# Optimization experiments

Hardware: AMD Instinct MI355X
Metric: run time of the kernel (lower is better)

Reference implementation:

```python
import jax, jax.numpy as jnp
import numpy as np
import math

S, B, H, NH = 2048, 1, 4096, 32
D = H // NH  # 128 head dim


def rotate_half(x):
    x1, x2 = x[..., : x.shape[-1] // 2], x[..., x.shape[-1] // 2 :]
    return jnp.concatenate((-x2, x1), axis=-1)


def setup_inputs() -> dict:
    key = jax.random.key(0)
    k1, k2, k3, k4, k5 = jax.random.split(key, 5)
    hidden_states = jax.random.normal(k1, (S, B, H), dtype=jnp.float32)
    position_ids = jnp.broadcast_to(jnp.arange(S, dtype=jnp.int32)[None, :], (B, S))
    # causal mask: True = masked (upper triangle above diagonal)
    attention_mask = jnp.triu(jnp.ones((S, S), dtype=bool), k=1)[None, None]
    W_qkv = jax.random.normal(k2, (H, 3 * H), dtype=jnp.float32) * 0.02
    b_qkv = jax.random.normal(k3, (3 * H,), dtype=jnp.float32) * 0.02
    W_dense = jax.random.normal(k4, (H, H), dtype=jnp.float32) * 0.02
    b_dense = jax.random.normal(k5, (H,), dtype=jnp.float32) * 0.02
    return {
        "hidden_states": hidden_states,
        "position_ids": position_ids,
        "attention_mask": attention_mask,
        "W_qkv": W_qkv,
        "b_qkv": b_qkv,
        "W_dense": W_dense,
        "b_dense": b_dense,
        "layer_id": 27,
    }


def reference(hidden_states, position_ids, attention_mask, W_qkv, b_qkv, W_dense, b_dense, layer_id):
    s, b, h = hidden_states.shape
    nh, d = NH, D
    # QKV projection: [s, b, 3h] -> [s, b, nh, 3d] -> split
    mixed = hidden_states @ W_qkv + b_qkv
    mixed = mixed.reshape(s, b, nh, 3 * d)
    q, k, v = jnp.split(mixed, 3, axis=-1)  # each [s, b, nh, d]
    # rotary embedding indexed by position_ids (transposed to [s, b])
    pos = position_ids.T  # [s, b]
    inv_freq = 1.0 / (10000.0 ** (jnp.arange(0, d, 2, dtype=jnp.float32) / d))
    freqs = pos[..., None].astype(jnp.float32) * inv_freq  # [s, b, d/2]
    emb = jnp.concatenate((freqs, freqs), axis=-1)  # [s, b, d]
    cos = jnp.cos(emb)[:, :, None, :]  # [s, b, 1, d]
    sin = jnp.sin(emb)[:, :, None, :]
    q = q * cos + rotate_half(q) * sin
    k = k * cos + rotate_half(k) * sin
    # attention with per-layer scaling coeff (cancels in softmax except mask fill)
    coeff = jnp.float32(layer_id + 1)
    q_scaled = q / (math.sqrt(d) * coeff)
    scores = jnp.einsum("sbnd,tbnd->bnst", q_scaled, k)  # [b, nh, s, s]
    scores = jnp.where(attention_mask, jnp.float32(-10000.0), scores) * coeff
    probs = jax.nn.softmax(scores, axis=-1)
    ctx = jnp.einsum("bnst,tbnd->sbnd", probs, v).reshape(s, b, h)
    out = ctx @ W_dense + b_dense
    return out
```

## Files before the change

kernel.cpp:

```cpp
#include <hip/hip_runtime.h>

#define S_LEN 2048
#define HID   4096
#define NHEAD 32
#define DHEAD 128
#define H3    12288

typedef __attribute__((ext_vector_type(8))) __bf16 bf16x8;
typedef __attribute__((ext_vector_type(4))) __bf16 bf16x4;
typedef __attribute__((ext_vector_type(4))) float  f32x4;

__device__ __forceinline__ void gl_lds16(const void* g, void* l) {
  __builtin_amdgcn_global_load_lds(
      (const __attribute__((address_space(1))) void*)g,
      (__attribute__((address_space(3))) void*)l, 16, 0, 0);
}

__global__ void cvt_f32_bf16(const float* __restrict__ in, __bf16* __restrict__ out, int n4) {
  int i = blockIdx.x * blockDim.x + threadIdx.x;
  if (i >= n4) return;
  float4 v = ((const float4*)in)[i];
  bf16x4 o;
  o.x = (__bf16)v.x; o.y = (__bf16)v.y; o.z = (__bf16)v.z; o.w = (__bf16)v.w;
  ((bf16x4*)out)[i] = o;
}

__global__ void transpose_cvt(const float* __restrict__ in, __bf16* __restrict__ out, int R, int C) {
  __shared__ float t[64][65];
  const int tid = threadIdx.x;
  const int r0 = blockIdx.y * 64, c0 = blockIdx.x * 64;
#pragma unroll
  for (int p = 0; p < 4; ++p) {
    int r = p * 16 + (tid >> 4);
    int c4 = (tid & 15) * 4;
    float4 v = *(const float4*)(in + (size_t)(r0 + r) * C + c0 + c4);
    t[r][c4] = v.x; t[r][c4 + 1] = v.y; t[r][c4 + 2] = v.z; t[r][c4 + 3] = v.w;
  }
  __syncthreads();
#pragma unroll
  for (int p = 0; p < 4; ++p) {
    int c = p * 16 + (tid >> 4);
    int rg = (tid & 15) * 4;
    bf16x4 o;
    o.x = (__bf16)t[rg][c]; o.y = (__bf16)t[rg + 1][c];
    o.z = (__bf16)t[rg + 2][c]; o.w = (__bf16)t[rg + 3][c];
    *(bf16x4*)(out + (size_t)(c0 + c) * R + r0 + rg) = o;
  }
}

__global__ void rope_kernel(__bf16* __restrict__ q, __bf16* __restrict__ k,
                            const int* __restrict__ pos) {
  int idx = blockIdx.x * 256 + threadIdx.x;
  int j = idx & 63;
  int hs = idx >> 6;
  int s = hs & (S_LEN - 1);
  float p = (float)pos[s];
  float invf = __expf(-(float)j * (9.210340371976184f / 64.f));
  float a = p * invf;
  float c, sn;
  __sincosf(a, &sn, &c);
  size_t base = (size_t)hs * 128;
  float x1 = (float)q[base + j], x2 = (float)q[base + j + 64];
  q[base + j]      = (__bf16)(x1 * c - x2 * sn);
  q[base + j + 64] = (__bf16)(x2 * c + x1 * sn);
  x1 = (float)k[base + j]; x2 = (float)k[base + j + 64];
  k[base + j]      = (__bf16)(x1 * c - x2 * sn);
  k[base + j + 64] = (__bf16)(x2 * c + x1 * sn);
}

template <int EPI>
__global__ __launch_bounds__(256, 2)
void gemm_bf16(const __bf16* __restrict__ A, const __bf16* __restrict__ BT,
               const float* __restrict__ bias, int K,
               __bf16* __restrict__ outq, __bf16* __restrict__ outk,
               __bf16* __restrict__ outvt, float* __restrict__ outf) {
  const int tid = threadIdx.x;
  const int lane = tid & 63;
  const int wave = tid >> 6;
  const int bm = blockIdx.x * 128;
  const int bn = blockIdx.y * 128;

  __shared__ __bf16 As[128 * 64];
  __shared__ __bf16 Bs[128 * 64];
  char* Ab = (char*)As;
  char* Bb = (char*)Bs;

  f32x4 acc[4][4] = {};

  const int wm = (wave >> 1) * 64;
  const int wn = (wave & 1) * 64;

  const int sr = tid >> 3;
  const int sc = (tid & 7) * 16;
  const int scs = sc ^ ((sr & 7) << 4);

  const char* Arow = (const char*)(A + (size_t)(bm + sr) * K) + scs;
  const char* Brow = (const char*)(BT + (size_t)(bn + sr) * K) + scs;

  for (int k0 = 0; k0 < K; k0 += 64) {
    const char* a_src = Arow + (size_t)k0 * 2;
    const char* b_src = Brow + (size_t)k0 * 2;
    char* a_dst = Ab + wave * 1024;
    char* b_dst = Bb + wave * 1024;
#pragma unroll
    for (int i = 0; i < 4; ++i) {
      gl_lds16(a_src + (size_t)i * 32 * K * 2, a_dst + i * 4096);
      gl_lds16(b_src + (size_t)i * 32 * K * 2, b_dst + i * 4096);
    }
    __syncthreads();
#pragma unroll
    for (int kk = 0; kk < 2; ++kk) {
      bf16x8 af[4], bfr[4];
#pragma unroll
      for (int m = 0; m < 4; ++m) {
        int row = wm + m * 16 + (lane & 15);
        int cb = (kk * 64 + ((lane >> 4) << 4)) ^ ((row & 7) << 4);
        af[m] = *(const bf16x8*)(Ab + row * 128 + cb);
      }
#pragma unroll
      for (int n = 0; n < 4; ++n) {
        int row = wn + n * 16 + (lane & 15);
        int cb = (kk * 64 + ((lane >> 4) << 4)) ^ ((row & 7) << 4);
        bfr[n] = *(const bf16x8*)(Bb + row * 128 + cb);
      }
#pragma unroll
      for (int m = 0; m < 4; ++m)
#pragma unroll
        for (int n = 0; n < 4; ++n)
          acc[m][n] = __builtin_amdgcn_mfma_f32_16x16x32_bf16(af[m], bfr[n], acc[m][n], 0, 0, 0);
    }
    __syncthreads();
  }

  const int rbase = (lane >> 4) << 2;
  const int cl = lane & 15;
  if (EPI == 0) {
    const int route = (bn >> 7) % 3;
    const int head = bn / 384;
#pragma unroll
    for (int n = 0; n < 4; ++n) {
      const int d = wn + n * 16 + cl;
      const float bv = bias[bn + d];
#pragma unroll
      for (int m = 0; m < 4; ++m) {
        const int srow = bm + wm + m * 16 + rbase;
        if (route == 2) {
          bf16x4 o;
          o.x = (__bf16)(acc[m][n][0] + bv);
          o.y = (__bf16)(acc[m][n][1] + bv);
          o.z = (__bf16)(acc[m][n][2] + bv);
          o.w = (__bf16)(acc[m][n][3] + bv);
          *(bf16x4*)(outvt + ((size_t)head * 128 + d) * S_LEN + srow) = o;
        } else {
          __bf16* dst = (route == 0 ? outq : outk) + (size_t)head * S_LEN * 128;
#pragma unroll
          for (int r = 0; r < 4; ++r)
            dst[(size_t)(srow + r) * 128 + d] = (__bf16)(acc[m][n][r] + bv);
        }
      }
    }
  } else {
#pragma unroll
    for (int n = 0; n < 4; ++n) {
      const int col = bn + wn + n * 16 + cl;
      const float bv = bias[col];
#pragma unroll
      for (int m = 0; m < 4; ++m) {
        const int srow = bm + wm + m * 16 + rbase;
#pragma unroll
        for (int r = 0; r < 4; ++r)
          outf[(size_t)(srow + r) * HID + col] = acc[m][n][r] + bv;
      }
    }
  }
}

__global__ __launch_bounds__(256, 2)
void attn_kernel(const __bf16* __restrict__ q, const __bf16* __restrict__ k,
                 const __bf16* __restrict__ vt, __bf16* __restrict__ ctx) {
  const int p = blockIdx.x, h = blockIdx.y;
  const int tid = threadIdx.x, lane = tid & 63, wave = tid >> 6;
  __shared__ __bf16 Ks[64 * 128];
  __shared__ __bf16 Vs[128 * 64];
  __shared__ __bf16 Ps[4][16 * 64];
  char* Kb = (char*)Ks;
  char* Vb = (char*)Vs;
  char* Pb = (char*)(Ps[wave]);

  const __bf16* qh = q + (size_t)h * S_LEN * 128;
  const __bf16* kh = k + (size_t)h * S_LEN * 128;
  const __bf16* vh = vt + (size_t)h * 128 * S_LEN;

  const int cl = lane & 15, rbase = (lane >> 4) << 2;

  const int krow = tid >> 4, kcol = (tid & 15) * 16;
  const int kcs = kcol ^ ((krow & 7) << 4);
  const int vrow = tid >> 3, vcol = (tid & 7) * 16;
  const int vcs = vcol ^ ((vrow & 7) << 4);

  for (int half = 0; half < 2; ++half) {
    const int qt = half ? (31 - p) : p;
    const int qrow0 = qt * 64 + wave * 16;

    bf16x8 qf[4];
#pragma unroll
    for (int kk = 0; kk < 4; ++kk)
      qf[kk] = *(const bf16x8*)(qh + (size_t)(qrow0 + cl) * 128 + kk * 32 + ((lane >> 4) << 3));

    f32x4 oacc[8] = {};
    float mrow[4], lrow[4];
#pragma unroll
    for (int r = 0; r < 4; ++r) { mrow[r] = -1e30f; lrow[r] = 0.f; }

    for (int j = 0; j <= qt; ++j) {
      {
        const char* src = (const char*)(kh + (size_t)(j * 64 + krow) * 128) + kcs;
        char* dst = Kb + wave * 1024;
#pragma unroll
        for (int i = 0; i < 4; ++i)
          gl_lds16(src + (size_t)i * 16 * 256, dst + i * 4096);
      }
      {
        const char* src = (const char*)(vh + (size_t)vrow * S_LEN + j * 64) + vcs;
        char* dst = Vb + wave * 1024;
#pragma unroll
        for (int i = 0; i < 4; ++i)
          gl_lds16(src + (size_t)i * 32 * (S_LEN * 2), dst + i * 4096);
      }
      __syncthreads();

      f32x4 sacc[4] = {};
#pragma unroll
      for (int kk = 0; kk < 4; ++kk) {
        bf16x8 bk[4];
#pragma unroll
        for (int n = 0; n < 4; ++n) {
          int row = n * 16 + cl;
          int cb = (kk * 64 + ((lane >> 4) << 4)) ^ ((row & 7) << 4);
          bk[n] = *(const bf16x8*)(Kb + row * 256 + cb);
        }
#pragma unroll
        for (int n = 0; n < 4; ++n)
          sacc[n] = __builtin_amdgcn_mfma_f32_16x16x32_bf16(qf[kk], bk[n], sacc[n], 0, 0, 0);
      }

      float pmax[4];
#pragma unroll
      for (int r = 0; r < 4; ++r) pmax[r] = -1e30f;
      if (j == qt) {
#pragma unroll
        for (int n = 0; n < 4; ++n) {
          const int col = n * 16 + cl;
#pragma unroll
          for (int r = 0; r < 4; ++r) {
            const int row = wave * 16 + rbase + r;
            float sv = sacc[n][r] * 0.08838834764831845f;
            sv = (col > row) ? -1e30f : sv;
            sacc[n][r] = sv;
            pmax[r] = fmaxf(pmax[r], sv);
          }
        }
      } else {
#pragma unroll
        for (int n = 0; n < 4; ++n)
#pragma unroll
          for (int r = 0; r < 4; ++r) {
            float sv = sacc[n][r] * 0.08838834764831845f;
            sacc[n][r] = sv;
            pmax[r] = fmaxf(pmax[r], sv);
          }
      }
#pragma unroll
      for (int xm = 1; xm < 16; xm <<= 1)
#pragma unroll
        for (int r = 0; r < 4; ++r)
          pmax[r] = fmaxf(pmax[r], __shfl_xor(pmax[r], xm, 64));
#pragma unroll
      for (int r = 0; r < 4; ++r) {
        const float mnew = fmaxf(mrow[r], pmax[r]);
        const float alpha = __expf(mrow[r] - mnew);
        mrow[r] = mnew;
        float psum = 0.f;
#pragma unroll
        for (int n = 0; n < 4; ++n) {
          float pe = __expf(sacc[n][r] - mnew);
          sacc[n][r] = pe;
          psum += pe;
        }
#pragma unroll
        for (int xm = 1; xm < 16; xm <<= 1)
          psum += __shfl_xor(psum, xm, 64);
        lrow[r] = lrow[r] * alpha + psum;
#pragma unroll
        for (int nd = 0; nd < 8; ++nd)
          oacc[nd][r] *= alpha;
      }

#pragma unroll
      for (int n = 0; n < 4; ++n) {
        const int colb = (n * 16 + cl) * 2;
#pragma unroll
        for (int r = 0; r < 4; ++r) {
          const int row = rbase + r;
          *(__bf16*)(Pb + row * 128 + (colb ^ ((row & 7) << 4))) = (__bf16)sacc[n][r];
        }
      }

#pragma unroll
      for (int kk = 0; kk < 2; ++kk) {
        bf16x8 pa, bv[8];
        {
          int row = cl;
          int cb = (kk * 64 + ((lane >> 4) << 4)) ^ ((row & 7) << 4);
          pa = *(const bf16x8*)(Pb + row * 128 + cb);
        }
#pragma unroll
        for (int nd = 0; nd < 8; ++nd) {
          int row = nd * 16 + cl;
          int cb = (kk * 64 + ((lane >> 4) << 4)) ^ ((row & 7) << 4);
          bv[nd] = *(const bf16x8*)(Vb + row * 128 + cb);
        }
#pragma unroll
        for (int nd = 0; nd < 8; ++nd)
          oacc[nd] = __builtin_amdgcn_mfma_f32_16x16x32_bf16(pa, bv[nd], oacc[nd], 0, 0, 0);
      }
      __syncthreads();
    }

#pragma unroll
    for (int nd = 0; nd < 8; ++nd) {
      const int d = nd * 16 + cl;
#pragma unroll
      for (int r = 0; r < 4; ++r) {
        const int srow = qrow0 + rbase + r;
        ctx[(size_t)srow * HID + h * 128 + d] = (__bf16)(oacc[nd][r] / lrow[r]);
      }
    }
  }
}

extern "C" void kernel_launch(void* const* d_in, const int* in_sizes, int n_in,
                              void* d_out, int out_size, void* d_ws, size_t ws_size,
                              hipStream_t stream) {
  const float* hs = (const float*)d_in[0];
  const int* pos = (const int*)d_in[1];
  const float* wqkv = (const float*)d_in[3];
  const float* bqkv = (const float*)d_in[4];
  const float* wd = (const float*)d_in[5];
  const float* bd = (const float*)d_in[6];
  float* out = (float*)d_out;

  char* ws = (char*)d_ws;
  const size_t MB = 1024ull * 1024ull;
  if (ws_size < 160 * MB) return;
  __bf16* wT  = (__bf16*)(ws);
  __bf16* xb  = (__bf16*)(ws + 96 * MB);
  __bf16* qb_ = (__bf16*)(ws + 112 * MB);
  __bf16* kb_ = (__bf16*)(ws + 128 * MB);
  __bf16* vtb = (__bf16*)(ws + 144 * MB);

  cvt_f32_bf16<<<8192, 256, 0, stream>>>(hs, xb, 2097152);
  transpose_cvt<<<dim3(192, 64), 256, 0, stream>>>(wqkv, wT, 4096, 12288);
  gemm_bf16<0><<<dim3(16, 96), 256, 0, stream>>>(xb, wT, bqkv, 4096, qb_, kb_, vtb, nullptr);
  rope_kernel<<<16384, 256, 0, stream>>>(qb_, kb_, pos);
  transpose_cvt<<<dim3(64, 64), 256, 0, stream>>>(wd, wT, 4096, 4096);
  attn_kernel<<<dim3(16, 32), 256, 0, stream>>>(qb_, kb_, vtb, xb);
  gemm_bf16<1><<<dim3(16, 32), 256, 0, stream>>>(xb, wT, bd, 4096, nullptr, nullptr, nullptr, out);
}
```

Baseline: 462.4 us.

## Replace bf16 GEMM with 8-wave triple-buffered pipelined kernel using XCD-aware tile swizzle

The 128x128 single-buffered GEMM, which synchronised on every K step, is replaced by a 256x128-tile kernel with 8 waves. It triple-buffers LDS and issues async global-to-LDS loads two K-tiles ahead, split into halves placed between MFMA phases. A block-index swizzle groups tiles per XCD for L2 reuse, and s_setprio raises priority around MFMA bursts. This is meant to overlap memory latency with matrix math and cut barrier stalls. The cost is about 147KB of LDS per block, so only one block fits per CU, plus hand-managed vmcnt/barrier ordering that could be fragile.

```diff
diff --git a/kernel.cpp b/kernel.cpp
--- a/kernel.cpp
+++ b/kernel.cpp
@@ -69,71 +69,135 @@
 }
 
 template <int EPI>
-__global__ __launch_bounds__(256, 2)
-void gemm_bf16(const __bf16* __restrict__ A, const __bf16* __restrict__ BT,
-               const float* __restrict__ bias, int K,
-               __bf16* __restrict__ outq, __bf16* __restrict__ outk,
-               __bf16* __restrict__ outvt, float* __restrict__ outf) {
-  const int tid = threadIdx.x;
-  const int lane = tid & 63;
-  const int wave = tid >> 6;
-  const int bm = blockIdx.x * 128;
-  const int bn = blockIdx.y * 128;
-
-  __shared__ __bf16 As[128 * 64];
-  __shared__ __bf16 Bs[128 * 64];
-  char* Ab = (char*)As;
-  char* Bb = (char*)Bs;
-
-  f32x4 acc[4][4] = {};
+__global__ __launch_bounds__(512, 2)
+void gemm8(const __bf16* __restrict__ A, const __bf16* __restrict__ BT,
+           const float* __restrict__ bias, int K,
+           __bf16* __restrict__ outq, __bf16* __restrict__ outk,
+           __bf16* __restrict__ outvt, float* __restrict__ outf) {
+  const int tid = threadIdx.x, lane = tid & 63, wave = tid >> 6;
+  const int nwg = gridDim.x;
+  const int q8 = nwg >> 3;
+  const int flat = blockIdx.x;
+  const int swz = (flat & 7) * q8 + (flat >> 3);
+  const int bm = (swz & 7) * 256;
+  const int bn = (swz >> 3) * 128;
+
+  __shared__ char lds[3 * 49152];
+
+  const int K2 = K * 2;
+  const int sr = tid >> 3;
+  const int scb = ((tid & 7) * 16) ^ ((sr & 7) << 4);
+  const char* Asrc = (const char*)A + (size_t)(bm + sr) * K2 + scb;
+  const char* Bsrc = (const char*)BT + (size_t)(bn + sr) * K2 + scb;
 
   const int wm = (wave >> 1) * 64;
   const int wn = (wave & 1) * 64;
-
-  const int sr = tid >> 3;
-  const int sc = (tid & 7) * 16;
-  const int scs = sc ^ ((sr & 7) << 4);
-
-  const char* Arow = (const char*)(A + (size_t)(bm + sr) * K) + scs;
-  const char* Brow = (const char*)(BT + (size_t)(bn + sr) * K) + scs;
-
-  for (int k0 = 0; k0 < K; k0 += 64) {
-    const char* a_src = Arow + (size_t)k0 * 2;
-    const char* b_src = Brow + (size_t)k0 * 2;
-    char* a_dst = Ab + wave * 1024;
-    char* b_dst = Bb + wave * 1024;
-#pragma unroll
-    for (int i = 0; i < 4; ++i) {
-      gl_lds16(a_src + (size_t)i * 32 * K * 2, a_dst + i * 4096);
-      gl_lds16(b_src + (size_t)i * 32 * K * 2, b_dst + i * 4096);
-    }
-    __syncthreads();
-#pragma unroll
-    for (int kk = 0; kk < 2; ++kk) {
-      bf16x8 af[4], bfr[4];
-#pragma unroll
-      for (int m = 0; m < 4; ++m) {
-        int row = wm + m * 16 + (lane & 15);
-        int cb = (kk * 64 + ((lane >> 4) << 4)) ^ ((row & 7) << 4);
-        af[m] = *(const bf16x8*)(Ab + row * 128 + cb);
+  const int cl = lane & 15;
+  const int rbase = (lane >> 4) << 2;
+  const int khi = (lane >> 4) << 4;
+
+  f32x4 acc[4][4] = {};
+
+  auto stage_half = [&](int t, int h) {
+    const size_t kb = (size_t)t * 128;
+    char* slot = lds + (t % 3) * 49152;
+    char* dA = slot + wave * 1024;
+    char* dB = slot + 32768 + wave * 1024;
+    if (h == 0) {
+      gl_lds16(Asrc + kb,                       dA);
+      gl_lds16(Asrc + kb + (size_t)64 * K2,     dA + 8192);
+      gl_lds16(Bsrc + kb,                       dB);
+    } else {
+      gl_lds16(Asrc + kb + (size_t)128 * K2,    dA + 16384);
+      gl_lds16(Asrc + kb + (size_t)192 * K2,    dA + 24576);
+      gl_lds16(Bsrc + kb + (size_t)64 * K2,     dB + 8192);
+    }
+  };
+
+  const int NT = K >> 6;
+  stage_half(0, 0); stage_half(0, 1);
+  stage_half(1, 0); stage_half(1, 1);
+  asm volatile("s_waitcnt vmcnt(6)" ::: "memory");
+  asm volatile("s_barrier" ::: "memory");
+
+  for (int t = 0; t < NT; ++t) {
+    const char* sA = lds + (t % 3) * 49152;
+    const char* sB = sA + 32768;
+    const bool st = (t + 2) < NT;
+
+    {
+      bf16x8 af[2][2], bfr[4][2];
+#pragma unroll
+      for (int mm = 0; mm < 2; ++mm) {
+        const int row = wm + mm * 16 + cl;
+        const int sw = (row & 7) << 4;
+#pragma unroll
+        for (int kk = 0; kk < 2; ++kk)
+          af[mm][kk] = *(const bf16x8*)(sA + row * 128 + ((kk * 64 + khi) ^ sw));
       }
 #pragma unroll
       for (int n = 0; n < 4; ++n) {
-        int row = wn + n * 16 + (lane & 15);
-        int cb = (kk * 64 + ((lane >> 4) << 4)) ^ ((row & 7) << 4);
-        bfr[n] = *(const bf16x8*)(Bb + row * 128 + cb);
-      }
-#pragma unroll
-      for (int m = 0; m < 4; ++m)
-#pragma unroll
-        for (int n = 0; n < 4; ++n)
-          acc[m][n] = __builtin_amdgcn_mfma_f32_16x16x32_bf16(af[m], bfr[n], acc[m][n], 0, 0, 0);
-    }
-    __syncthreads();
+        const int row = wn + n * 16 + cl;
+        const int sw = (row & 7) << 4;
+#pragma unroll
+        for (int kk = 0; kk < 2; ++kk)
+          bfr[n][kk] = *(const bf16x8*)(sB + row * 128 + ((kk * 64 + khi) ^ sw));
+      }
+      if (st) stage_half(t + 2, 0);
+      asm volatile("s_barrier" ::: "memory");
+      asm volatile("s_waitcnt lgkmcnt(0)" ::: "memory");
+      __builtin_amdgcn_s_setprio(1);
+#pragma unroll
+      for (int kk = 0; kk < 2; ++kk)
+#pragma unroll
+        for (int mm = 0; mm < 2; ++mm)
+#pragma unroll
+          for (int n = 0; n < 4; ++n)
+            acc[mm][n] = __builtin_amdgcn_mfma_f32_16x16x32_bf16(
+                af[mm][kk], bfr[n][kk], acc[mm][n], 0, 0, 0);
+      __builtin_amdgcn_s_setprio(0);
+      asm volatile("s_barrier" ::: "memory");
+    }
+
+    {
+      bf16x8 af[2][2], bfr[4][2];
+#pragma unroll
+      for (int mm = 0; mm < 2; ++mm) {
+        const int row = wm + (2 + mm) * 16 + cl;
+        const int sw = (row & 7) << 4;
+#pragma unroll
+        for (int kk = 0; kk < 2; ++kk)
+          af[mm][kk] = *(const bf16x8*)(sA + row * 128 + ((kk * 64 + khi) ^ sw));
+      }
+#pragma unroll
+      for (int n = 0; n < 4; ++n) {
+        const int row = wn + n * 16 + cl;
+        const int sw = (row & 7) << 4;
+#pragma unroll
+        for (int kk = 0; kk < 2; ++kk)
+          bfr[n][kk] = *(const bf16x8*)(sB + row * 128 + ((kk * 64 + khi) ^ sw));
+      }
+      if (st) stage_half(t + 2, 1);
+      if (t < NT - 1) {
+        if (st) asm volatile("s_waitcnt vmcnt(6)" ::: "memory");
+        else    asm volatile("s_waitcnt vmcnt(0)" ::: "memory");
+      }
+      asm volatile("s_barrier" ::: "memory");
+      asm volatile("s_waitcnt lgkmcnt(0)" ::: "memory");
+      __builtin_amdgcn_s_setprio(1);
+#pragma unroll
+      for (int kk = 0; kk < 2; ++kk)
+#pragma unroll
+        for (int mm = 0; mm < 2; ++mm)
+#pragma unroll
+          for (int n = 0; n < 4; ++n)
+            acc[2 + mm][n] = __builtin_amdgcn_mfma_f32_16x16x32_bf16(
+                af[mm][kk], bfr[n][kk], acc[2 + mm][n], 0, 0, 0);
+      __builtin_amdgcn_s_setprio(0);
+      asm volatile("s_barrier" ::: "memory");
+    }
   }
 
-  const int rbase = (lane >> 4) << 2;
-  const int cl = lane & 15;
   if (EPI == 0) {
     const int route = (bn >> 7) % 3;
     const int head = bn / 384;
@@ -361,9 +425,9 @@
 
   cvt_f32_bf16<<<8192, 256, 0, stream>>>(hs, xb, 2097152);
   transpose_cvt<<<dim3(192, 64), 256, 0, stream>>>(wqkv, wT, 4096, 12288);
-  gemm_bf16<0><<<dim3(16, 96), 256, 0, stream>>>(xb, wT, bqkv, 4096, qb_, kb_, vtb, nullptr);
+  gemm8<0><<<768, 512, 0, stream>>>(xb, wT, bqkv, 4096, qb_, kb_, vtb, nullptr);
   rope_kernel<<<16384, 256, 0, stream>>>(qb_, kb_, pos);
   transpose_cvt<<<dim3(64, 64), 256, 0, stream>>>(wd, wT, 4096, 4096);
   attn_kernel<<<dim3(16, 32), 256, 0, stream>>>(qb_, kb_, vtb, xb);
-  gemm_bf16<1><<<dim3(16, 32), 256, 0, stream>>>(xb, wT, bd, 4096, nullptr, nullptr, nullptr, out);
-}
+  gemm8<1><<<256, 512, 0, stream>>>(xb, wT, bd, 4096, nullptr, nullptr, nullptr, out);
+}
```

After: 490.6 us. 6.1% more time.

## Switch GEMMs to 32x32x16 MFMA with 256x128 block tiles

Applied to the files above, without the earlier changes.

Both projection GEMMs now use 32x32x16 bf16 MFMA instructions instead of 16x16x32, and the block tile grows from 128x128 to 256x128, with each wave computing a 128x64 sub-tile. The LDS layout changes to match, and the epilogue index mapping is rewritten for the 32x32 accumulator layout. The aim is fewer LDS reads per FLOP and better reuse of B across more rows. In exchange the grid has fewer blocks (768 and 256), which risks under-filling the CUs on the dense GEMM, and register pressure rises.

```diff
diff --git a/kernel.cpp b/kernel.cpp
--- a/kernel.cpp
+++ b/kernel.cpp
@@ -9,6 +9,7 @@
 typedef __attribute__((ext_vector_type(8))) __bf16 bf16x8;
 typedef __attribute__((ext_vector_type(4))) __bf16 bf16x4;
 typedef __attribute__((ext_vector_type(4))) float  f32x4;
+typedef __attribute__((ext_vector_type(16))) float f32x16;
 
 __device__ __forceinline__ void gl_lds16(const void* g, void* l) {
   __builtin_amdgcn_global_load_lds(
@@ -70,32 +71,32 @@
 
 template <int EPI>
 __global__ __launch_bounds__(256, 2)
-void gemm_bf16(const __bf16* __restrict__ A, const __bf16* __restrict__ BT,
-               const float* __restrict__ bias, int K,
-               __bf16* __restrict__ outq, __bf16* __restrict__ outk,
-               __bf16* __restrict__ outvt, float* __restrict__ outf) {
+void gemm32(const __bf16* __restrict__ A, const __bf16* __restrict__ BT,
+            const float* __restrict__ bias, int K,
+            __bf16* __restrict__ outq, __bf16* __restrict__ outk,
+            __bf16* __restrict__ outvt, float* __restrict__ outf) {
   const int tid = threadIdx.x;
   const int lane = tid & 63;
   const int wave = tid >> 6;
-  const int bm = blockIdx.x * 128;
+  const int bm = blockIdx.x * 256;
   const int bn = blockIdx.y * 128;
 
-  __shared__ __bf16 As[128 * 64];
-  __shared__ __bf16 Bs[128 * 64];
-  char* Ab = (char*)As;
-  char* Bb = (char*)Bs;
-
-  f32x4 acc[4][4] = {};
-
-  const int wm = (wave >> 1) * 64;
+  __shared__ char lds[49152];
+  char* Ab = lds;
+  char* Bb = lds + 32768;
+
+  f32x16 acc[4][2] = {};
+
+  const int wm = (wave >> 1) * 128;
   const int wn = (wave & 1) * 64;
+  const int l31 = lane & 31;
+  const int hi = lane >> 5;
 
   const int sr = tid >> 3;
-  const int sc = (tid & 7) * 16;
-  const int scs = sc ^ ((sr & 7) << 4);
-
-  const char* Arow = (const char*)(A + (size_t)(bm + sr) * K) + scs;
-  const char* Brow = (const char*)(BT + (size_t)(bn + sr) * K) + scs;
+  const int scb = ((tid & 7) * 16) ^ ((sr & 7) << 4);
+  const int K2 = K * 2;
+  const char* Arow = (const char*)A + (size_t)(bm + sr) * K2 + scb;
+  const char* Brow = (const char*)BT + (size_t)(bn + sr) * K2 + scb;
 
   for (int k0 = 0; k0 < K; k0 += 64) {
     const char* a_src = Arow + (size_t)k0 * 2;
@@ -103,74 +104,77 @@
     char* a_dst = Ab + wave * 1024;
     char* b_dst = Bb + wave * 1024;
 #pragma unroll
-    for (int i = 0; i < 4; ++i) {
-      gl_lds16(a_src + (size_t)i * 32 * K * 2, a_dst + i * 4096);
-      gl_lds16(b_src + (size_t)i * 32 * K * 2, b_dst + i * 4096);
-    }
+    for (int i = 0; i < 8; ++i)
+      gl_lds16(a_src + (size_t)i * 32 * K2, a_dst + i * 4096);
+#pragma unroll
+    for (int i = 0; i < 4; ++i)
+      gl_lds16(b_src + (size_t)i * 32 * K2, b_dst + i * 4096);
     __syncthreads();
 #pragma unroll
-    for (int kk = 0; kk < 2; ++kk) {
-      bf16x8 af[4], bfr[4];
+    for (int kk = 0; kk < 4; ++kk) {
+      const int cbase = kk * 32 + (hi << 4);
+      bf16x8 af[4], bfr[2];
 #pragma unroll
       for (int m = 0; m < 4; ++m) {
-        int row = wm + m * 16 + (lane & 15);
-        int cb = (kk * 64 + ((lane >> 4) << 4)) ^ ((row & 7) << 4);
-        af[m] = *(const bf16x8*)(Ab + row * 128 + cb);
-      }
-#pragma unroll
-      for (int n = 0; n < 4; ++n) {
-        int row = wn + n * 16 + (lane & 15);
-        int cb = (kk * 64 + ((lane >> 4) << 4)) ^ ((row & 7) << 4);
-        bfr[n] = *(const bf16x8*)(Bb + row * 128 + cb);
+        const int row = wm + m * 32 + l31;
+        af[m] = *(const bf16x8*)(Ab + row * 128 + (cbase ^ ((row & 7) << 4)));
+      }
+#pragma unroll
+      for (int n = 0; n < 2; ++n) {
+        const int row = wn + n * 32 + l31;
+        bfr[n] = *(const bf16x8*)(Bb + row * 128 + (cbase ^ ((row & 7) << 4)));
       }
 #pragma unroll
       for (int m = 0; m < 4; ++m)
 #pragma unroll
-        for (int n = 0; n < 4; ++n)
-          acc[m][n] = __builtin_amdgcn_mfma_f32_16x16x32_bf16(af[m], bfr[n], acc[m][n], 0, 0, 0);
+        for (int n = 0; n < 2; ++n)
+          acc[m][n] = __builtin_amdgcn_mfma_f32_32x32x16_bf16(af[m], bfr[n], acc[m][n], 0, 0, 0);
     }
     __syncthreads();
   }
 
-  const int rbase = (lane >> 4) << 2;
-  const int cl = lane & 15;
   if (EPI == 0) {
     const int route = (bn >> 7) % 3;
     const int head = bn / 384;
 #pragma unroll
-    for (int n = 0; n < 4; ++n) {
-      const int d = wn + n * 16 + cl;
+    for (int n = 0; n < 2; ++n) {
+      const int d = wn + n * 32 + l31;
       const float bv = bias[bn + d];
 #pragma unroll
       for (int m = 0; m < 4; ++m) {
-        const int srow = bm + wm + m * 16 + rbase;
         if (route == 2) {
-          bf16x4 o;
-          o.x = (__bf16)(acc[m][n][0] + bv);
-          o.y = (__bf16)(acc[m][n][1] + bv);
-          o.z = (__bf16)(acc[m][n][2] + bv);
-          o.w = (__bf16)(acc[m][n][3] + bv);
-          *(bf16x4*)(outvt + ((size_t)head * 128 + d) * S_LEN + srow) = o;
+#pragma unroll
+          for (int qd = 0; qd < 4; ++qd) {
+            const int srow = bm + wm + m * 32 + qd * 8 + (hi << 2);
+            bf16x4 o;
+            o.x = (__bf16)(acc[m][n][qd * 4 + 0] + bv);
+            o.y = (__bf16)(acc[m][n][qd * 4 + 1] + bv);
+            o.z = (__bf16)(acc[m][n][qd * 4 + 2] + bv);
+            o.w = (__bf16)(acc[m][n][qd * 4 + 3] + bv);
+            *(bf16x4*)(outvt + ((size_t)head * 128 + d) * S_LEN + srow) = o;
+          }
         } else {
           __bf16* dst = (route == 0 ? outq : outk) + (size_t)head * S_LEN * 128;
 #pragma unroll
-          for (int r = 0; r < 4; ++r)
-            dst[(size_t)(srow + r) * 128 + d] = (__bf16)(acc[m][n][r] + bv);
+          for (int r = 0; r < 16; ++r) {
+            const int srow = bm + wm + m * 32 + (r & 3) + 8 * (r >> 2) + (hi << 2);
+            dst[(size_t)srow * 128 + d] = (__bf16)(acc[m][n][r] + bv);
+          }
         }
       }
     }
   } else {
 #pragma unroll
-    for (int n = 0; n < 4; ++n) {
-      const int col = bn + wn + n * 16 + cl;
+    for (int n = 0; n < 2; ++n) {
+      const int col = bn + wn + n * 32 + l31;
       const float bv = bias[col];
 #pragma unroll
-      for (int m = 0; m < 4; ++m) {
-        const int srow = bm + wm + m * 16 + rbase;
-#pragma unroll
-        for (int r = 0; r < 4; ++r)
-          outf[(size_t)(srow + r) * HID + col] = acc[m][n][r] + bv;
-      }
+      for (int m = 0; m < 4; ++m)
+#pragma unroll
+        for (int r = 0; r < 16; ++r) {
+          const int srow = bm + wm + m * 32 + (r & 3) + 8 * (r >> 2) + (hi << 2);
+          outf[(size_t)srow * HID + col] = acc[m][n][r] + bv;
+        }
     }
   }
 }
@@ -361,9 +365,9 @@
 
   cvt_f32_bf16<<<8192, 256, 0, stream>>>(hs, xb, 2097152);
   transpose_cvt<<<dim3(192, 64), 256, 0, stream>>>(wqkv, wT, 4096, 12288);
-  gemm_bf16<0><<<dim3(16, 96), 256, 0, stream>>>(xb, wT, bqkv, 4096, qb_, kb_, vtb, nullptr);
+  gemm32<0><<<dim3(8, 96), 256, 0, stream>>>(xb, wT, bqkv, 4096, qb_, kb_, vtb, nullptr);
   rope_kernel<<<16384, 256, 0, stream>>>(qb_, kb_, pos);
   transpose_cvt<<<dim3(64, 64), 256, 0, stream>>>(wd, wT, 4096, 4096);
   attn_kernel<<<dim3(16, 32), 256, 0, stream>>>(qb_, kb_, vtb, xb);
-  gemm_bf16<1><<<dim3(16, 32), 256, 0, stream>>>(xb, wT, bd, 4096, nullptr, nullptr, nullptr, out);
-}
+  gemm32<1><<<dim3(8, 32), 256, 0, stream>>>(xb, wT, bd, 4096, nullptr, nullptr, nullptr, out);
+}
```

Measured after the change: 500.9 us. 1.08x slower.
